# Optimization experiments

Hardware: AMD Instinct MI355X
Metric: run time of the kernel (lower is better)

The kernel has to match this reference:

```python
import jax, jax.numpy as jnp
import numpy as np


def setup_inputs() -> dict:
    key = jax.random.key(0)
    k1, k2 = jax.random.split(key)
    B, C, H, W = 16, 32, 256, 256
    OH, OW = 256, 256
    Im = jax.random.normal(k1, (B, C, H, W), dtype=jnp.float32)
    # pixel-space sampling coordinates in [0, W-1] / [0, H-1]
    gx = jax.random.uniform(k2, (B, 1, OH, OW), dtype=jnp.float32) * (W - 1)
    gy = jax.random.uniform(jax.random.fold_in(k2, 1), (B, 1, OH, OW), dtype=jnp.float32) * (H - 1)
    G = jnp.concatenate([gx, gy], axis=1)  # [B, 2, OH, OW]
    return {"Im": Im, "G": G}


def reference(Im, G):
    # replicate-pad by 1 on each spatial side
    Imp = jnp.pad(Im, ((0, 0), (0, 0), (1, 1), (1, 1)), mode='edge')
    B, C, H, W = Imp.shape
    _, _, OH, OW = G.shape
    # flatten coords per batch; +1 accounts for the pad
    x = G[:, 0].reshape(B, -1) + 1.0  # [B, OH*OW]
    y = G[:, 1].reshape(B, -1) + 1.0
    max_x, max_y = W - 1, H - 1
    x0 = jnp.floor(x).astype(jnp.int32)
    y0 = jnp.floor(y).astype(jnp.int32)
    x1 = x0 + 1
    y1 = y0 + 1
    x0 = jnp.clip(x0, 0, max_x)
    x1 = jnp.clip(x1, 0, max_x)
    y0 = jnp.clip(y0, 0, max_y)
    y1 = jnp.clip(y1, 0, max_y)
    # [B, H*W, C] channels-last flat image, gather per batch
    Im_flat = Imp.transpose(0, 2, 3, 1).reshape(B, H * W, C)

    def gather(yi, xi):
        idx = yi * W + xi  # [B, OH*OW]
        return jnp.take_along_axis(Im_flat, idx[:, :, None], axis=1)  # [B, OH*OW, C]

    Ia = gather(y0, x0)
    Ib = gather(y1, x0)
    Ic = gather(y0, x1)
    Id = gather(y1, x1)
    dx = x1.astype(jnp.float32) - x  # note: uses clamped x1, as in the original
    dy = y1.astype(jnp.float32) - y
    wa = (dy * dx)[:, :, None]
    wb = ((1.0 - dy) * dx)[:, :, None]
    wc = (dy * (1.0 - dx))[:, :, None]
    wd = ((1.0 - dy) * (1.0 - dx))[:, :, None]
    out = wa * Ia + wb * Ib + wc * Ic + wd * Id  # [B, OH*OW, C]
    return out.reshape(B, OH, OW, C).transpose(0, 3, 1, 2)
```

## Files before the change

kernel.cpp:

```cpp
#include <hip/hip_runtime.h>

#define BB 16
#define CC 32
#define HH 256
#define WW 256
#define OHH 256
#define OWW 256
#define HW  (HH * WW)

typedef _Float16 half8 __attribute__((ext_vector_type(8)));
typedef _Float16 half4v __attribute__((ext_vector_type(4)));

__global__ __launch_bounds__(256) void nchw_to_nhwc_h(
    const float* __restrict__ Im,
    _Float16* __restrict__ dst)
{
    __shared__ float lds[64 * 33];
    int blk = blockIdx.x;
    int wt = blk & 3;
    int h  = (blk >> 2) & (HH - 1);
    int b  = blk >> 10;
    int w0 = wt * 64;
    int t  = threadIdx.x;

    const float* src = Im + ((size_t)b * CC * HH + h) * WW;

    #pragma unroll
    for (int i = 0; i < 2; ++i) {
        int idx = i * 256 + t;
        int c  = idx >> 4;
        int wq = (idx & 15) * 4;
        float4 v = *(const float4*)(src + (size_t)c * HW + w0 + wq);
        lds[(wq + 0) * 33 + c] = v.x;
        lds[(wq + 1) * 33 + c] = v.y;
        lds[(wq + 2) * 33 + c] = v.z;
        lds[(wq + 3) * 33 + c] = v.w;
    }
    __syncthreads();

    _Float16* dstp = dst + (((size_t)b * HH + h) * WW + w0) * CC;
    #pragma unroll
    for (int i = 0; i < 2; ++i) {
        int idx = i * 256 + t;
        int w  = idx >> 3;
        int c4 = (idx & 7) * 4;
        half4v v;
        v.x = (_Float16)lds[w * 33 + c4 + 0];
        v.y = (_Float16)lds[w * 33 + c4 + 1];
        v.z = (_Float16)lds[w * 33 + c4 + 2];
        v.w = (_Float16)lds[w * 33 + c4 + 3];
        *(half4v*)(dstp + w * CC + c4) = v;
    }
}

__global__ __launch_bounds__(256) void bilerp_gather_h(
    const _Float16* __restrict__ img,
    const float* __restrict__ G,
    float* __restrict__ out)
{
    int tid = blockIdx.x * blockDim.x + threadIdx.x;
    int hid = tid & 1;
    int pix = tid >> 1;
    int ox = pix & (OWW - 1);
    int oy = (pix >> 8) & (OHH - 1);
    int b  = pix >> 16;

    const float* Gb = G + (size_t)b * 2 * HW + oy * OWW + ox;
    float gx = Gb[0];
    float gy = Gb[HW];

    float x = gx + 1.0f;
    float y = gy + 1.0f;
    int x0 = (int)floorf(x);
    int y0 = (int)floorf(y);
    int x1 = x0 + 1;
    int y1 = y0 + 1;
    x0 = min(max(x0, 0), WW + 1);
    x1 = min(max(x1, 0), WW + 1);
    y0 = min(max(y0, 0), HH + 1);
    y1 = min(max(y1, 0), HH + 1);
    float dx = (float)x1 - x;
    float dy = (float)y1 - y;

    int xi0 = min(max(x0 - 1, 0), WW - 1);
    int xi1 = min(max(x1 - 1, 0), WW - 1);
    int yi0 = min(max(y0 - 1, 0), HH - 1);
    int yi1 = min(max(y1 - 1, 0), HH - 1);

    float wa = dy * dx;
    float wb = (1.0f - dy) * dx;
    float wc = dy * (1.0f - dx);
    float wd = (1.0f - dy) * (1.0f - dx);

    const _Float16* base = img + (size_t)b * HW * CC + hid * 16;
    const half8* pa = (const half8*)(base + ((size_t)yi0 * WW + xi0) * CC);
    const half8* pb = (const half8*)(base + ((size_t)yi1 * WW + xi0) * CC);
    const half8* pc = (const half8*)(base + ((size_t)yi0 * WW + xi1) * CC);
    const half8* pd = (const half8*)(base + ((size_t)yi1 * WW + xi1) * CC);

    half8 a0 = pa[0], a1 = pa[1];
    half8 b0 = pb[0], b1 = pb[1];
    half8 c0 = pc[0], c1 = pc[1];
    half8 d0 = pd[0], d1 = pd[1];

    float r[16];
    #pragma unroll
    for (int j = 0; j < 8; ++j) {
        r[j]     = wa * (float)a0[j] + wb * (float)b0[j]
                 + wc * (float)c0[j] + wd * (float)d0[j];
        r[j + 8] = wa * (float)a1[j] + wb * (float)b1[j]
                 + wc * (float)c1[j] + wd * (float)d1[j];
    }

    float* outp = out + ((size_t)b * CC + hid * 16) * HW + oy * OWW + ox;
    #pragma unroll
    for (int j = 0; j < 16; ++j) {
        outp[j * HW] = r[j];
    }
}

__global__ __launch_bounds__(256) void bilerp_direct(
    const float* __restrict__ Im, const float* __restrict__ G,
    float* __restrict__ out)
{
    int idx = blockIdx.x * blockDim.x + threadIdx.x;
    int ox = idx & (OWW - 1);
    int oy = (idx >> 8) & (OHH - 1);
    int b  = idx >> 16;

    const float* Gb = G + (size_t)b * 2 * HW + oy * OWW + ox;
    float x = Gb[0] + 1.0f;
    float y = Gb[HW] + 1.0f;
    int x0 = (int)floorf(x), y0 = (int)floorf(y);
    int x1 = x0 + 1, y1 = y0 + 1;
    x0 = min(max(x0, 0), WW + 1); x1 = min(max(x1, 0), WW + 1);
    y0 = min(max(y0, 0), HH + 1); y1 = min(max(y1, 0), HH + 1);
    float dx = (float)x1 - x, dy = (float)y1 - y;
    int xi0 = min(max(x0 - 1, 0), WW - 1), xi1 = min(max(x1 - 1, 0), WW - 1);
    int yi0 = min(max(y0 - 1, 0), HH - 1), yi1 = min(max(y1 - 1, 0), HH - 1);
    float wa = dy * dx, wb = (1.0f - dy) * dx;
    float wc = dy * (1.0f - dx), wd = (1.0f - dy) * (1.0f - dx);

    const float* Ibase = Im + (size_t)b * CC * HW;
    int o00 = yi0 * WW + xi0, o01 = yi0 * WW + xi1;
    int o10 = yi1 * WW + xi0, o11 = yi1 * WW + xi1;
    float* outp = out + (size_t)b * CC * HW + oy * OWW + ox;
    #pragma unroll 4
    for (int c = 0; c < CC; ++c) {
        const float* p = Ibase + c * HW;
        outp[c * HW] = wa * p[o00] + wb * p[o10] + wc * p[o01] + wd * p[o11];
    }
}

extern "C" void kernel_launch(void* const* d_in, const int* in_sizes, int n_in,
                              void* d_out, int out_size, void* d_ws, size_t ws_size,
                              hipStream_t stream) {
    const float* Im = (const float*)d_in[0];
    const float* G  = (const float*)d_in[1];
    float* out = (float*)d_out;

    const size_t needed = (size_t)BB * HW * CC * sizeof(_Float16);
    int total = BB * OHH * OWW;

    if (ws_size >= needed) {
        _Float16* nhwc = (_Float16*)d_ws;
        nchw_to_nhwc_h<<<dim3(BB * HH * (WW / 64)), dim3(256), 0, stream>>>(Im, nhwc);
        bilerp_gather_h<<<dim3(2 * total / 256), dim3(256), 0, stream>>>(nhwc, G, out);
    } else {
        bilerp_direct<<<dim3(total / 256), dim3(256), 0, stream>>>(Im, G, out);
    }
}
```

Baseline: 283.3 us.

## Remap blocks to keep each batch on one XCD and use nontemporal streaming accesses

Result: faster. 267.4 us (-5.6%).

```diff
diff --git a/kernel.cpp b/kernel.cpp
--- a/kernel.cpp
+++ b/kernel.cpp
@@ -10,17 +10,20 @@
 
 typedef _Float16 half8 __attribute__((ext_vector_type(8)));
 typedef _Float16 half4v __attribute__((ext_vector_type(4)));
+typedef float float4v __attribute__((ext_vector_type(4)));
 
 __global__ __launch_bounds__(256) void nchw_to_nhwc_h(
     const float* __restrict__ Im,
     _Float16* __restrict__ dst)
 {
     __shared__ float lds[64 * 33];
-    int blk = blockIdx.x;
-    int wt = blk & 3;
-    int h  = (blk >> 2) & (HH - 1);
-    int b  = blk >> 10;
-    int w0 = wt * 64;
+    int blk  = blockIdx.x;
+    int xcd  = blk & 7;
+    int slot = blk >> 3;
+    int b    = xcd + 8 * (slot >> 10);
+    int inner = slot & 1023;
+    int h  = inner >> 2;
+    int w0 = (inner & 3) * 64;
     int t  = threadIdx.x;
 
     const float* src = Im + ((size_t)b * CC * HH + h) * WW;
@@ -30,7 +33,8 @@
         int idx = i * 256 + t;
         int c  = idx >> 4;
         int wq = (idx & 15) * 4;
-        float4 v = *(const float4*)(src + (size_t)c * HW + w0 + wq);
+        float4v v = __builtin_nontemporal_load(
+            (const float4v*)(src + (size_t)c * HW + w0 + wq));
         lds[(wq + 0) * 33 + c] = v.x;
         lds[(wq + 1) * 33 + c] = v.y;
         lds[(wq + 2) * 33 + c] = v.z;
@@ -58,16 +62,20 @@
     const float* __restrict__ G,
     float* __restrict__ out)
 {
-    int tid = blockIdx.x * blockDim.x + threadIdx.x;
-    int hid = tid & 1;
-    int pix = tid >> 1;
-    int ox = pix & (OWW - 1);
-    int oy = (pix >> 8) & (OHH - 1);
-    int b  = pix >> 16;
+    int blk  = blockIdx.x;
+    int xcd  = blk & 7;
+    int slot = blk >> 3;
+    int b    = xcd + 8 * (1 - (slot >> 9));
+    int inner = slot & 511;
+    int t    = threadIdx.x;
+    int hid  = t & 1;
+    int pixb = inner * 128 + (t >> 1);
+    int ox = pixb & (OWW - 1);
+    int oy = pixb >> 8;
 
     const float* Gb = G + (size_t)b * 2 * HW + oy * OWW + ox;
-    float gx = Gb[0];
-    float gy = Gb[HW];
+    float gx = __builtin_nontemporal_load(Gb);
+    float gy = __builtin_nontemporal_load(Gb + HW);
 
     float x = gx + 1.0f;
     float y = gy + 1.0f;
@@ -115,7 +123,7 @@
     float* outp = out + ((size_t)b * CC + hid * 16) * HW + oy * OWW + ox;
     #pragma unroll
     for (int j = 0; j < 16; ++j) {
-        outp[j * HW] = r[j];
+        __builtin_nontemporal_store(r[j], outp + j * HW);
     }
 }
 
```
